# Kernel tuning notes

Hardware: AMD Instinct MI355X
Metric: run time of the kernel (lower is better)

Reference implementation:

```python
import jax, jax.numpy as jnp
import numpy as np

B, T, V, S = 32, 2048, 1024, 256
BLANK = 0
NEG = -1e30  # log-space 'zero' (avoids inf so zero_infinity handling is a simple threshold)


def setup_inputs() -> dict:
    key = jax.random.key(0)
    k1, k2, k3, k4 = jax.random.split(key, 4)
    # valid log-probabilities, as produced by an upstream log_softmax head
    preds_logprob = jax.nn.log_softmax(
        jax.random.normal(k1, (B, T, V), dtype=jnp.float32), axis=-1)
    tokens_gt = jax.random.randint(k2, (B, S), 1, V)            # labels exclude blank=0
    cqt_lens = jax.random.randint(k3, (B,), T // 2, T + 1)      # input lengths
    token_lens_gt = jax.random.randint(k4, (B,), S // 2, S + 1) # target lengths (>=1)
    return {"preds_logprob": preds_logprob, "tokens_gt": tokens_gt,
            "cqt_lens": cqt_lens, "token_lens_gt": token_lens_gt}


def _ctc_single(lp, ext, rep_ok, Tl, Sl):
    """Negative CTC log-likelihood for one sample.
    lp: [T, V] log-probs; ext: [L=2S+1] extended label seq (blanks interleaved);
    rep_ok: [L] bool, whether the s-2 -> s skip transition is allowed;
    Tl: input length; Sl: target length (>=1)."""
    emit = lp[:, ext]  # [T, L] emission log-probs, gathered once outside the scan
    L = ext.shape[0]
    alpha = jnp.full((L,), NEG, dtype=lp.dtype)
    alpha = alpha.at[0].set(emit[0, 0]).at[1].set(emit[0, 1])

    neg1 = jnp.full((1,), NEG, dtype=lp.dtype)
    neg2 = jnp.full((2,), NEG, dtype=lp.dtype)

    def step(alpha, xs):
        e, t = xs
        a1 = jnp.concatenate([neg1, alpha[:-1]])
        a2 = jnp.concatenate([neg2, alpha[:-2]])
        a2 = jnp.where(rep_ok, a2, NEG)
        m = jnp.maximum(jnp.maximum(alpha, a1), a2)
        new = e + m + jnp.log(jnp.exp(alpha - m) + jnp.exp(a1 - m) + jnp.exp(a2 - m))
        # freeze the lattice past this sample's input length (masking by cqt_lens)
        alpha = jnp.where(t < Tl, new, alpha)
        return alpha, None

    ts = jnp.arange(1, lp.shape[0])
    alpha, _ = jax.lax.scan(step, alpha, (emit[1:], ts))

    # log-likelihood = logsumexp over the two terminal lattice states
    lA = alpha[2 * Sl]
    lB = alpha[2 * Sl - 1]
    m = jnp.maximum(lA, lB)
    ll = m + jnp.log(jnp.exp(lA - m) + jnp.exp(lB - m))
    return -ll


def _ctc_loss(preds_logprob, tokens_gt, cqt_lens, token_lens_gt):
    # mask_by_length: zero out frames past cqt_lens (no effect on CTC value,
    # kept for faithfulness); swapaxes(0,1) is a pure layout change.
    tmask = jnp.arange(T)[None, :] < cqt_lens[:, None]          # [B, T]
    lp = preds_logprob * tmask[:, :, None].astype(preds_logprob.dtype)

    # extended label sequence with blanks interleaved: [blank, y1, blank, ..., yS, blank]
    ext = jnp.zeros((B, 2 * S + 1), dtype=tokens_gt.dtype).at[:, 1::2].set(tokens_gt)
    ext_m2 = jnp.concatenate([jnp.zeros((B, 2), dtype=ext.dtype), ext[:, :-2]], axis=1)
    rep_ok = (ext != BLANK) & (ext != ext_m2)                   # allow s-2 skip

    losses = jax.vmap(_ctc_single)(lp, ext, rep_ok, cqt_lens, token_lens_gt)  # [B]
    # zero_infinity=True: unreachable alignments produce ~ -NEG; zero them out
    losses = jnp.where(losses > 1e29, 0.0, losses)
    # reduction='mean': divide by target length, then mean over batch
    return jnp.mean(losses / token_lens_gt.astype(losses.dtype))


def reference(preds_logprob, tokens_gt, cqt_lens, token_lens_gt):
    return _ctc_loss(preds_logprob, tokens_gt, cqt_lens, token_lens_gt)
```

## Files before the change

### kernel.cpp

```cpp
#include <hip/hip_runtime.h>
#include <math.h>

#define BB 32
#define TT 2048
#define VV 1024
#define SS 256
#define TCHUNK 4
#define NSLOT 6

__device__ __forceinline__ void async_ld16(const float* g, const float* l) {
    __builtin_amdgcn_global_load_lds(
        (const __attribute__((address_space(1))) void*)(uintptr_t)g,
        (__attribute__((address_space(3))) void*)(unsigned)(uintptr_t)l, 16, 0, 0);
}
__device__ __forceinline__ void async_ld4(const float* g, const float* l) {
    __builtin_amdgcn_global_load_lds(
        (const __attribute__((address_space(1))) void*)(uintptr_t)g,
        (__attribute__((address_space(3))) void*)(unsigned)(uintptr_t)l, 4, 0, 0);
}
#define WAIT_VM0() __builtin_amdgcn_s_waitcnt(0x0F70)

__device__ __forceinline__ float dpp_shr1_f(float x) {
    int r = __builtin_amdgcn_update_dpp(0, __float_as_int(x), 0x138, 0xF, 0xF, true);
    return __int_as_float(r);
}
__device__ __forceinline__ int dpp_shr1_i(int x) {
    return __builtin_amdgcn_update_dpp(0, x, 0x138, 0xF, 0xF, true);
}

__global__ __launch_bounds__(256) void ctc_pre(const float* __restrict__ lp,
    const int* __restrict__ tokens, const int* __restrict__ cqt,
    const int* __restrict__ slen, float* __restrict__ G, float* __restrict__ Gbl,
    float* __restrict__ out)
{
    __shared__ __align__(16) float rows[TCHUNK][VV];
    __shared__ int toks[SS];
    const int tid = threadIdx.x;
    const int bx  = blockIdx.x;
    if (bx == 0 && tid == 0) out[0] = 0.f;
    const int nchunk = TT / TCHUNK;
    const int b  = bx / nchunk;
    const int t0 = (bx % nchunk) * TCHUNK;
    const int Tl = cqt[b];
    if (t0 >= Tl) return;
    const int Sl = slen[b];
    toks[tid] = tokens[b * SS + tid];
#pragma unroll
    for (int k = 0; k < TCHUNK; ++k) {
        const int t = t0 + k;
        if (t < Tl)
            ((float4*)rows[k])[tid] = ((const float4*)(lp + ((size_t)b * TT + t) * VV))[tid];
    }
    __syncthreads();
#pragma unroll
    for (int k = 0; k < TCHUNK; ++k) {
        const int t = t0 + k;
        if (t >= Tl) break;
        float* gp = G + ((size_t)b * TT + t) * 256;
        gp[tid] = (tid < Sl) ? __expf(rows[k][toks[tid]]) : 0.f;
        if (tid == 0) Gbl[b * TT + t] = __expf(rows[k][0]);
    }
}

__global__ __launch_bounds__(256) void ctc_walk(const float* __restrict__ G,
    const float* __restrict__ Gbl, const int* __restrict__ tokens,
    const int* __restrict__ cqt, const int* __restrict__ slen, float* __restrict__ out)
{
    __shared__ __align__(16) float tokL[NSLOT][8 * 256];
    __shared__ __align__(16) float blkL[NSLOT][64];
    __shared__ float als[513];
    __shared__ int   aE[65];
    __shared__ int   ready[NSLOT];
    __shared__ int   prog;

    const int b    = blockIdx.x;
    const int tid  = threadIdx.x;
    const int wid  = tid >> 6;
    const int lane = tid & 63;
    const int Tl   = cqt[b];
    const float* __restrict__ Gb   = G   + (size_t)b * TT * 256;
    const float* __restrict__ GblB = Gbl + (size_t)b * TT;

    if (tid < NSLOT) ready[tid] = -1;
    if (tid == NSLOT) prog = -1;
    __syncthreads();

    const int NC = (Tl + 6) >> 3;
    volatile int* vready = ready;
    volatile int* vprog  = &prog;

    if (wid != 0) {
        for (int c = wid - 1; c < NC; c += 3) {
            const int slot = c % NSLOT;
            while (*vprog < c - NSLOT) {}
            __builtin_amdgcn_sched_barrier(0);
            asm volatile("" ::: "memory");
            const int tbase = 1 + (c << 3);
            const float* lt = tokL[slot];
#pragma unroll
            for (int k = 0; k < 8; ++k) {
                int tt = tbase + k; tt = (tt < Tl) ? tt : (Tl - 1);
                async_ld16(Gb + (size_t)tt * 256 + (lane << 2), lt + k * 256);
            }
            int tbk = tbase + lane; tbk = (tbk < Tl) ? tbk : (Tl - 1);
            async_ld4(GblB + tbk, blkL[slot]);
            WAIT_VM0();
            __builtin_amdgcn_sched_barrier(0);
            asm volatile("" ::: "memory");
            vready[slot] = c;
        }
        return;
    }

    const int Sl = slen[b];
    const int j0 = lane * 4;
    const int* tb = tokens + b * SS;
    const int tm1 = (j0 == 0) ? 0 : tb[j0 - 1];
    const int q0 = tb[j0], q1 = tb[j0 + 1], q2 = tb[j0 + 2], q3 = tb[j0 + 3];
    const float m0 = (q0 != tm1) ? 1.f : 0.f;
    const float m1 = (q1 != q0)  ? 1.f : 0.f;
    const float m2 = (q2 != q1)  ? 1.f : 0.f;
    const float m3 = (q3 != q2)  ? 1.f : 0.f;
    const float lzm = (lane == 0) ? 0.f : 1.f;

    float a0=0.f,a1=0.f,a2=0.f,a3=0.f,a4=0.f,a5=0.f,a6=0.f,a7=0.f,aX=0.f;
    if (lane == 0) { a0 = GblB[0]; a1 = Gb[0]; }
    int   Etot = 0;
    float sfac = lzm;

#define LOADCHUNK(s) do { \
    _Pragma("unroll") \
    for (int k = 0; k < 8; ++k) { \
        pr[k] = ((const float4*)(tokL[s] + (k << 8)))[lane]; \
        pb[k] = blkL[s][k]; \
    } \
} while (0)

#define ONESTEP(P4, PB) do { \
    const float pb_ = (PB); \
    const float h1 = dpp_shr1_f(a7) * sfac; \
    const float n0 = pb_ * (a0 + h1); \
    const float n1 = (P4).x * (a1 + a0 + m0 * h1); \
    const float n2 = pb_ * (a2 + a1); \
    const float n3 = (P4).y * (a3 + a2 + m1 * a1); \
    const float n4 = pb_ * (a4 + a3); \
    const float n5 = (P4).z * (a5 + a4 + m2 * a3); \
    const float n6 = pb_ * (a6 + a5); \
    const float n7 = (P4).w * (a7 + a6 + m3 * a5); \
    aX = pb_ * (aX + a7); \
    a0=n0;a1=n1;a2=n2;a3=n3;a4=n4;a5=n5;a6=n6;a7=n7; \
} while (0)

#define RENORM_LOCAL() do { \
    float mm = fmaxf(fmaxf(fmaxf(a0,a1),fmaxf(a2,a3)), fmaxf(fmaxf(a4,a5),fmaxf(a6,a7))); \
    mm = fmaxf(mm, aX); \
    int ee = (__float_as_int(mm) >> 23) - 126; \
    ee = (mm > 0.f) ? ee : 0; \
    const float sc = __int_as_float((127 - ee) << 23); \
    a0*=sc;a1*=sc;a2*=sc;a3*=sc;a4*=sc;a5*=sc;a6*=sc;a7*=sc;aX*=sc; \
    Etot += ee; \
    int Ep = dpp_shr1_i(Etot); \
    if (mm == 0.f && lane > 0) Etot = Ep; \
    Ep = dpp_shr1_i(Etot); \
    if (mm == 0.f && lane > 0) Etot = Ep; \
    int dd = Ep - Etot; \
    dd = (dd < -126) ? -126 : ((dd > 100) ? 100 : dd); \
    sfac = __int_as_float((127 + dd) << 23) * lzm; \
} while (0)

    float4 pr[8];
    float  pb[8];

    const int F = (Tl - 1) >> 3;
    for (int c = 0; c < F; ++c) {
        const int slot = c % NSLOT;
        while (vready[slot] < c) {}
        __builtin_amdgcn_sched_barrier(0);
        asm volatile("" ::: "memory");
        LOADCHUNK(slot);
        asm volatile("" ::: "memory");
        *vprog = c;
#pragma unroll
        for (int k = 0; k < 8; ++k) {
            ONESTEP(pr[k], pb[k]);
            if (k == 3 || k == 7) RENORM_LOCAL();
        }
    }
    if (F < NC) {
        const int slot = F % NSLOT;
        while (vready[slot] < F) {}
        __builtin_amdgcn_sched_barrier(0);
        asm volatile("" ::: "memory");
        LOADCHUNK(slot);
        asm volatile("" ::: "memory");
        *vprog = F;
        const int nv = (Tl - 1) - (F << 3);
#pragma unroll
        for (int k = 0; k < 8; ++k) {
            if (k < nv) ONESTEP(pr[k], pb[k]);
            if (k == 3 || k == 7) RENORM_LOCAL();
        }
    }

    als[8 * lane + 0] = a0; als[8 * lane + 1] = a1;
    als[8 * lane + 2] = a2; als[8 * lane + 3] = a3;
    als[8 * lane + 4] = a4; als[8 * lane + 5] = a5;
    als[8 * lane + 6] = a6; als[8 * lane + 7] = a7;
    aE[lane] = Etot;
    if (lane == 63) { als[512] = aX; aE[64] = Etot; }
    asm volatile("s_waitcnt lgkmcnt(0)" ::: "memory");
    if (lane == 0) {
        const int sA = 2 * Sl, sB = 2 * Sl - 1;
        const float vA = als[sA], vB = als[sB];
        const int   eA = aE[sA >> 3], eB = aE[sB >> 3];
        int em;
        if (vA > 0.f && vB > 0.f) em = (eA > eB) ? eA : eB;
        else if (vA > 0.f)        em = eA;
        else if (vB > 0.f)        em = eB;
        else                      em = 0;
        const double s = ldexp((double)vA, eA - em) + ldexp((double)vB, eB - em);
        double loss = -(log(s) + (double)em * 0.6931471805599453);
        if (!(loss < 1e29)) loss = 0.0;
        atomicAdd(out, (float)(loss / ((double)Sl * (double)BB)));
    }
#undef LOADCHUNK
#undef ONESTEP
#undef RENORM_LOCAL
}

extern "C" void kernel_launch(void* const* d_in, const int* in_sizes, int n_in,
                              void* d_out, int out_size, void* d_ws, size_t ws_size,
                              hipStream_t stream)
{
    const float* lp     = (const float*)d_in[0];
    const int*   tokens = (const int*)d_in[1];
    const int*   cqt    = (const int*)d_in[2];
    const int*   slen   = (const int*)d_in[3];
    float* out = (float*)d_out;
    float* G   = (float*)d_ws;
    float* Gbl = G + (size_t)BB * TT * 256;

    hipLaunchKernelGGL(ctc_pre,  dim3(BB * (TT / TCHUNK)), dim3(256), 0, stream,
                       lp, tokens, cqt, slen, G, Gbl, out);
    hipLaunchKernelGGL(ctc_walk, dim3(BB), dim3(256), 0, stream,
                       G, Gbl, tokens, cqt, slen, out);
}
```

Baseline: 519.1 us.

## Factor blank emission out of CTC recurrence and enlarge walk chunks

The pre-pass now stores each token emission divided by that frame's blank probability, plus the raw blank log-prob. The walk therefore skips multiplying the five blank-lattice states by the blank probability on every step, and the summed blank log-probs are added back to the loss in double precision at the end. The walk also moves from 8-step chunks with 6 slots to 16-step chunks with 3 fixed slots, one per producer wave, and uses v_max3 for the renormalisation max. The risk is that the emission ratios can grow large, which relies on the existing exponent renormalisation every 4 steps to stay in range.

```diff
diff --git a/kernel.cpp b/kernel.cpp
--- a/kernel.cpp
+++ b/kernel.cpp
@@ -6,7 +6,8 @@
 #define VV 1024
 #define SS 256
 #define TCHUNK 4
-#define NSLOT 6
+#define CH 16
+#define NSLOT 3
 
 __device__ __forceinline__ void async_ld16(const float* g, const float* l) {
     __builtin_amdgcn_global_load_lds(
@@ -26,6 +27,11 @@
 }
 __device__ __forceinline__ int dpp_shr1_i(int x) {
     return __builtin_amdgcn_update_dpp(0, x, 0x138, 0xF, 0xF, true);
+}
+__device__ __forceinline__ float max3f(float a, float b, float c) {
+    float d;
+    asm("v_max3_f32 %0, %1, %2, %3" : "=v"(d) : "v"(a), "v"(b), "v"(c));
+    return d;
 }
 
 __global__ __launch_bounds__(256) void ctc_pre(const float* __restrict__ lp,
@@ -56,9 +62,10 @@
     for (int k = 0; k < TCHUNK; ++k) {
         const int t = t0 + k;
         if (t >= Tl) break;
+        const float pb0 = rows[k][0];
         float* gp = G + ((size_t)b * TT + t) * 256;
-        gp[tid] = (tid < Sl) ? __expf(rows[k][toks[tid]]) : 0.f;
-        if (tid == 0) Gbl[b * TT + t] = __expf(rows[k][0]);
+        gp[tid] = (tid < Sl) ? __expf(rows[k][toks[tid]] - pb0) : 0.f;
+        if (tid == 0) Gbl[b * TT + t] = pb0;
     }
 }
 
@@ -66,7 +73,7 @@
     const float* __restrict__ Gbl, const int* __restrict__ tokens,
     const int* __restrict__ cqt, const int* __restrict__ slen, float* __restrict__ out)
 {
-    __shared__ __align__(16) float tokL[NSLOT][8 * 256];
+    __shared__ __align__(16) float tokL[NSLOT][CH * 256];
     __shared__ __align__(16) float blkL[NSLOT][64];
     __shared__ float als[513];
     __shared__ int   aE[65];
@@ -85,20 +92,20 @@
     if (tid == NSLOT) prog = -1;
     __syncthreads();
 
-    const int NC = (Tl + 6) >> 3;
+    const int NC = (Tl + 14) >> 4;
     volatile int* vready = ready;
     volatile int* vprog  = &prog;
 
     if (wid != 0) {
+        const int slot = wid - 1;
         for (int c = wid - 1; c < NC; c += 3) {
-            const int slot = c % NSLOT;
             while (*vprog < c - NSLOT) {}
             __builtin_amdgcn_sched_barrier(0);
             asm volatile("" ::: "memory");
-            const int tbase = 1 + (c << 3);
+            const int tbase = 1 + (c << 4);
             const float* lt = tokL[slot];
 #pragma unroll
-            for (int k = 0; k < 8; ++k) {
+            for (int k = 0; k < CH; ++k) {
                 int tt = tbase + k; tt = (tt < Tl) ? tt : (Tl - 1);
                 async_ld16(Gb + (size_t)tt * 256 + (lane << 2), lt + k * 256);
             }
@@ -124,36 +131,39 @@
     const float lzm = (lane == 0) ? 0.f : 1.f;
 
     float a0=0.f,a1=0.f,a2=0.f,a3=0.f,a4=0.f,a5=0.f,a6=0.f,a7=0.f,aX=0.f;
-    if (lane == 0) { a0 = GblB[0]; a1 = Gb[0]; }
-    int   Etot = 0;
-    float sfac = lzm;
+    if (lane == 0) {
+        const float e0 = __expf(GblB[0]);
+        a0 = e0;
+        a1 = Gb[0] * e0;
+    }
+    int    Etot = 0;
+    float  sfac = lzm;
+    double bacc = 0.0;
 
 #define LOADCHUNK(s) do { \
     _Pragma("unroll") \
-    for (int k = 0; k < 8; ++k) { \
+    for (int k = 0; k < CH; ++k) { \
         pr[k] = ((const float4*)(tokL[s] + (k << 8)))[lane]; \
         pb[k] = blkL[s][k]; \
     } \
 } while (0)
 
-#define ONESTEP(P4, PB) do { \
-    const float pb_ = (PB); \
+#define ONESTEP(P4) do { \
     const float h1 = dpp_shr1_f(a7) * sfac; \
-    const float n0 = pb_ * (a0 + h1); \
+    const float n0 = a0 + h1; \
     const float n1 = (P4).x * (a1 + a0 + m0 * h1); \
-    const float n2 = pb_ * (a2 + a1); \
+    const float n2 = a2 + a1; \
     const float n3 = (P4).y * (a3 + a2 + m1 * a1); \
-    const float n4 = pb_ * (a4 + a3); \
+    const float n4 = a4 + a3; \
     const float n5 = (P4).z * (a5 + a4 + m2 * a3); \
-    const float n6 = pb_ * (a6 + a5); \
+    const float n6 = a6 + a5; \
     const float n7 = (P4).w * (a7 + a6 + m3 * a5); \
-    aX = pb_ * (aX + a7); \
+    aX = aX + a7; \
     a0=n0;a1=n1;a2=n2;a3=n3;a4=n4;a5=n5;a6=n6;a7=n7; \
 } while (0)
 
 #define RENORM_LOCAL() do { \
-    float mm = fmaxf(fmaxf(fmaxf(a0,a1),fmaxf(a2,a3)), fmaxf(fmaxf(a4,a5),fmaxf(a6,a7))); \
-    mm = fmaxf(mm, aX); \
+    const float mm = max3f(max3f(a0,a1,a2), max3f(a3,a4,a5), max3f(a6,a7,aX)); \
     int ee = (__float_as_int(mm) >> 23) - 126; \
     ee = (mm > 0.f) ? ee : 0; \
     const float sc = __int_as_float((127 - ee) << 23); \
@@ -168,38 +178,38 @@
     sfac = __int_as_float((127 + dd) << 23) * lzm; \
 } while (0)
 
-    float4 pr[8];
-    float  pb[8];
-
-    const int F = (Tl - 1) >> 3;
-    for (int c = 0; c < F; ++c) {
-        const int slot = c % NSLOT;
+    float4 pr[CH];
+    float  pb[CH];
+
+    const int F = (Tl - 1) >> 4;
+    int slot = 0;
+    for (int c = 0; c < NC; ++c) {
         while (vready[slot] < c) {}
         __builtin_amdgcn_sched_barrier(0);
         asm volatile("" ::: "memory");
         LOADCHUNK(slot);
         asm volatile("" ::: "memory");
         *vprog = c;
-#pragma unroll
-        for (int k = 0; k < 8; ++k) {
-            ONESTEP(pr[k], pb[k]);
-            if (k == 3 || k == 7) RENORM_LOCAL();
+        if (c < F) {
+            float bt = ((pb[0]+pb[1])+(pb[2]+pb[3]))+((pb[4]+pb[5])+(pb[6]+pb[7]));
+            bt += ((pb[8]+pb[9])+(pb[10]+pb[11]))+((pb[12]+pb[13])+(pb[14]+pb[15]));
+            bacc += (double)bt;
+#pragma unroll
+            for (int k = 0; k < CH; ++k) {
+                ONESTEP(pr[k]);
+                if ((k & 3) == 3) RENORM_LOCAL();
+            }
+        } else {
+            const int nv = (Tl - 1) - (F << 4);
+            float bt = 0.f;
+#pragma unroll
+            for (int k = 0; k < CH; ++k) {
+                if (k < nv) { bt += pb[k]; ONESTEP(pr[k]); }
+                if ((k & 3) == 3) RENORM_LOCAL();
+            }
+            bacc += (double)bt;
         }
-    }
-    if (F < NC) {
-        const int slot = F % NSLOT;
-        while (vready[slot] < F) {}
-        __builtin_amdgcn_sched_barrier(0);
-        asm volatile("" ::: "memory");
-        LOADCHUNK(slot);
-        asm volatile("" ::: "memory");
-        *vprog = F;
-        const int nv = (Tl - 1) - (F << 3);
-#pragma unroll
-        for (int k = 0; k < 8; ++k) {
-            if (k < nv) ONESTEP(pr[k], pb[k]);
-            if (k == 3 || k == 7) RENORM_LOCAL();
-        }
+        slot = (slot == NSLOT - 1) ? 0 : slot + 1;
     }
 
     als[8 * lane + 0] = a0; als[8 * lane + 1] = a1;
@@ -219,7 +229,7 @@
         else if (vB > 0.f)        em = eB;
         else                      em = 0;
         const double s = ldexp((double)vA, eA - em) + ldexp((double)vB, eB - em);
-        double loss = -(log(s) + (double)em * 0.6931471805599453);
+        double loss = -(log(s) + (double)em * 0.6931471805599453 + bacc);
         if (!(loss < 1e29)) loss = 0.0;
         atomicAdd(out, (float)(loss / ((double)Sl * (double)BB)));
     }
```

Result: faster. 486.0 us (-6.4%).
